# Kernel optimization log

Hardware: AMD Instinct MI355X
Metric: run time of the kernel (lower is better)

Reference implementation:

```python
import jax, jax.numpy as jnp
import numpy as np

N_ENV, N_STEP = 4096, 2048
GAMMA, LAMBDA = 0.99, 0.95


def setup_inputs() -> dict:
    key = jax.random.key(0)
    k1, k2, k3 = jax.random.split(key, 3)
    rewards = jax.random.normal(k1, (N_ENV, N_STEP), dtype=jnp.float32)
    values = jax.random.normal(k2, (N_ENV, N_STEP + 1), dtype=jnp.float32)
    first = (jax.random.uniform(k3, (N_ENV, N_STEP + 1)) < 0.01).astype(jnp.float32)
    return {"rewards": rewards, "values": values, "first": first}


def reference(rewards, values, first):
    """GAE backward recurrence, vectorized over envs via a reverse lax.scan.

    advantages[t] = delta[t] + notlast[t]*gamma*lambda*advantages[t+1]
    delta[t]      = r[t] + notlast[t]*gamma*V[t+1] - V[t]
    """
    notlast = 1.0 - first[:, 1:]                        # [E, T]
    delta = rewards + notlast * GAMMA * values[:, 1:] - values[:, :-1]  # [E, T]

    def step(lastgaelam, xs):
        d_t, nl_t = xs                                  # each [E]
        adv_t = d_t + nl_t * (GAMMA * LAMBDA) * lastgaelam
        return adv_t, adv_t

    init = jnp.zeros(rewards.shape[0], dtype=rewards.dtype)
    _, advs = jax.lax.scan(step, init, (delta.T, notlast.T), reverse=True)
    advantages = advs.T                                 # [E, T]
    v_targ = values[:, :-1] + advantages
    return advantages, v_targ
```

## Files before the change

### kernel.cpp

```cpp
#include <hip/hip_runtime.h>


constexpr int NE   = 4096;
constexpr int NT   = 2048;
constexpr int NT1  = 2049;
constexpr float GAMMA  = 0.99f;
constexpr float LAMBDA = 0.95f;
constexpr int TPB = 256;
constexpr int PER = NT / TPB;
constexpr int NQ  = NT / 4;
constexpr int QPT = NQ / TPB;

typedef float f32x4 __attribute__((ext_vector_type(4)));
typedef float f32x4u __attribute__((ext_vector_type(4), aligned(4)));

__device__ __forceinline__ f32x4 ld4u(const float* p) {
    return (f32x4)*reinterpret_cast<const f32x4u*>(p);
}

__device__ __forceinline__ int swz(int g) { return g ^ ((g >> 3) & 7); }

__global__ __launch_bounds__(TPB) void gae_kernel(
    const float* __restrict__ rewards,
    const float* __restrict__ values,
    const float* __restrict__ first,
    float* __restrict__ out)
{
    __shared__ f32x4 d_lds[NQ];
    __shared__ f32x4 c_lds[NQ];
    __shared__ float sWA[4];
    __shared__ float sWB[4];

    const int e    = blockIdx.x;
    const int tid  = threadIdx.x;
    const int lane = tid & 63;
    const int w    = tid >> 6;

    const float* r_row = rewards + (size_t)e * NT;
    const float* v_row = values  + (size_t)e * NT1;
    const float* f_row = first   + (size_t)e * NT1;

    f32x4 vreg[QPT];
#pragma unroll
    for (int j = 0; j < QPT; ++j) {
        const int q = j * TPB + tid;
        const int t = 4 * q;
        const f32x4 r4  = *reinterpret_cast<const f32x4*>(r_row + t);
        const f32x4 v4a = ld4u(v_row + t);
        const f32x4 v4b = ld4u(v_row + t + 1);
        const f32x4 f4  = ld4u(f_row + t + 1);
        vreg[j] = v4a;
        const f32x4 nl = 1.0f - f4;
        f32x4 d4, c4;
        d4 = r4 + nl * GAMMA * v4b - v4a;
        c4 = nl * (GAMMA * LAMBDA);
        d_lds[swz(q)] = d4;
        c_lds[swz(q)] = c4;
    }
    __syncthreads();

    float d[PER], c[PER];
    {
        const f32x4 da = d_lds[swz(2 * tid)];
        const f32x4 db = d_lds[swz(2 * tid + 1)];
        const f32x4 ca = c_lds[swz(2 * tid)];
        const f32x4 cb = c_lds[swz(2 * tid + 1)];
        d[0]=da.x; d[1]=da.y; d[2]=da.z; d[3]=da.w;
        d[4]=db.x; d[5]=db.y; d[6]=db.z; d[7]=db.w;
        c[0]=ca.x; c[1]=ca.y; c[2]=ca.z; c[3]=ca.w;
        c[4]=cb.x; c[5]=cb.y; c[6]=cb.z; c[7]=cb.w;
    }

    float A = 1.0f, B = 0.0f;
#pragma unroll
    for (int k = PER - 1; k >= 0; --k) {
        B = fmaf(c[k], B, d[k]);
        A *= c[k];
    }

    float cA = A, cB = B;
#pragma unroll
    for (int off = 1; off < 64; off <<= 1) {
        const float a2 = __shfl_down(cA, off);
        const float b2 = __shfl_down(cB, off);
        if (lane + off < 64) {
            cB = fmaf(cA, b2, cB);
            cA = cA * a2;
        }
    }

    if (lane == 0) { sWA[w] = cA; sWB[w] = cB; }

    float EA = __shfl_down(cA, 1);
    float EB = __shfl_down(cB, 1);
    if (lane == 63) { EA = 1.0f; EB = 0.0f; }

    __syncthreads();

    float TB = 0.0f;
    for (int u = 3; u > w; --u) {
        TB = fmaf(sWA[u], TB, sWB[u]);
    }
    float x = fmaf(EA, TB, EB);

    float adv[PER];
#pragma unroll
    for (int k = PER - 1; k >= 0; --k) {
        x = fmaf(c[k], x, d[k]);
        adv[k] = x;
    }
    {
        f32x4 a0; a0.x=adv[0]; a0.y=adv[1]; a0.z=adv[2]; a0.w=adv[3];
        f32x4 a1; a1.x=adv[4]; a1.y=adv[5]; a1.z=adv[6]; a1.w=adv[7];
        d_lds[swz(2 * tid)]     = a0;
        d_lds[swz(2 * tid + 1)] = a1;
    }
    __syncthreads();

    float* __restrict__ adv_out = out + (size_t)e * NT;
    float* __restrict__ vt_out  = out + (size_t)NE * NT + (size_t)e * NT;
#pragma unroll
    for (int j = 0; j < QPT; ++j) {
        const int q = j * TPB + tid;
        const int t = 4 * q;
        const f32x4 a4 = d_lds[swz(q)];
        const f32x4 vt = vreg[j] + a4;
        __builtin_nontemporal_store(a4, reinterpret_cast<f32x4*>(adv_out + t));
        __builtin_nontemporal_store(vt, reinterpret_cast<f32x4*>(vt_out + t));
    }
}

extern "C" void kernel_launch(void* const* d_in, const int* in_sizes, int n_in,
                              void* d_out, int out_size, void* d_ws, size_t ws_size,
                              hipStream_t stream) {
    const float* rewards = (const float*)d_in[0];
    const float* values  = (const float*)d_in[1];
    const float* first   = (const float*)d_in[2];
    float* out = (float*)d_out;
    gae_kernel<<<NE, TPB, 0, stream>>>(rewards, values, first, out);
}
```

Before: 30.01 us.

## Process two envs per block, prefetching second env's loads during first's scan

Each block now handles two environment rows. The second row's global loads are issued before the first row's scan runs, so memory latency overlaps with compute. The shifted values load is replaced by a cross-lane shuffle plus one scalar load for the last lane. __syncthreads is swapped for a raw barrier that waits only on LDS counters. The cost is roughly doubled register pressure from holding the prefetched row, which may lower occupancy, and half as many blocks are launched.

Result: no change. 30.49 us (+1.6%).

```diff
diff --git a/kernel.cpp b/kernel.cpp
--- a/kernel.cpp
+++ b/kernel.cpp
@@ -10,6 +10,8 @@
 constexpr int PER = NT / TPB;
 constexpr int NQ  = NT / 4;
 constexpr int QPT = NQ / TPB;
+constexpr int EPB = 2;
+constexpr int NB  = NE / EPB;
 
 typedef float f32x4 __attribute__((ext_vector_type(4)));
 typedef float f32x4u __attribute__((ext_vector_type(4), aligned(4)));
@@ -20,45 +22,52 @@
 
 __device__ __forceinline__ int swz(int g) { return g ^ ((g >> 3) & 7); }
 
-__global__ __launch_bounds__(TPB) void gae_kernel(
-    const float* __restrict__ rewards,
-    const float* __restrict__ values,
-    const float* __restrict__ first,
-    float* __restrict__ out)
+__device__ __forceinline__ void bar_lds() {
+    asm volatile("s_waitcnt lgkmcnt(0)" ::: "memory");
+    __builtin_amdgcn_sched_barrier(0);
+    __builtin_amdgcn_s_barrier();
+    __builtin_amdgcn_sched_barrier(0);
+}
+
+struct Env { f32x4 r[QPT], v[QPT], f[QPT]; float vn[QPT]; };
+
+__device__ __forceinline__ void load_env(int e, int tid, int lane,
+    const float* __restrict__ rewards, const float* __restrict__ values,
+    const float* __restrict__ first, Env& E)
 {
-    __shared__ f32x4 d_lds[NQ];
-    __shared__ f32x4 c_lds[NQ];
-    __shared__ float sWA[4];
-    __shared__ float sWB[4];
-
-    const int e    = blockIdx.x;
-    const int tid  = threadIdx.x;
-    const int lane = tid & 63;
-    const int w    = tid >> 6;
-
     const float* r_row = rewards + (size_t)e * NT;
     const float* v_row = values  + (size_t)e * NT1;
     const float* f_row = first   + (size_t)e * NT1;
+#pragma unroll
+    for (int j = 0; j < QPT; ++j) {
+        const int t = 4 * (j * TPB + tid);
+        E.r[j] = *reinterpret_cast<const f32x4*>(r_row + t);
+        E.v[j] = ld4u(v_row + t);
+        E.f[j] = ld4u(f_row + t + 1);
+        E.vn[j] = (lane == 63) ? v_row[t + 4] : 0.0f;
+    }
+}
 
-    f32x4 vreg[QPT];
+__device__ __forceinline__ void phase1(const Env& E, int tid, int lane,
+    f32x4* d_lds, f32x4* c_lds, f32x4 vreg[QPT])
+{
 #pragma unroll
     for (int j = 0; j < QPT; ++j) {
         const int q = j * TPB + tid;
-        const int t = 4 * q;
-        const f32x4 r4  = *reinterpret_cast<const f32x4*>(r_row + t);
-        const f32x4 v4a = ld4u(v_row + t);
-        const f32x4 v4b = ld4u(v_row + t + 1);
-        const f32x4 f4  = ld4u(f_row + t + 1);
-        vreg[j] = v4a;
-        const f32x4 nl = 1.0f - f4;
-        f32x4 d4, c4;
-        d4 = r4 + nl * GAMMA * v4b - v4a;
-        c4 = nl * (GAMMA * LAMBDA);
-        d_lds[swz(q)] = d4;
-        c_lds[swz(q)] = c4;
+        float vnext = __shfl_down(E.v[j].x, 1);
+        if (lane == 63) vnext = E.vn[j];
+        f32x4 v4b; v4b.x = E.v[j].y; v4b.y = E.v[j].z; v4b.z = E.v[j].w; v4b.w = vnext;
+        const f32x4 nl = 1.0f - E.f[j];
+        d_lds[swz(q)] = E.r[j] + nl * GAMMA * v4b - E.v[j];
+        c_lds[swz(q)] = nl * (GAMMA * LAMBDA);
+        vreg[j] = E.v[j];
     }
-    __syncthreads();
+}
 
+__device__ __forceinline__ void phase23(int e, int tid, int lane, int w,
+    f32x4* d_lds, f32x4* c_lds, float* sWA, float* sWB,
+    const f32x4 vreg[QPT], float* __restrict__ out)
+{
     float d[PER], c[PER];
     {
         const f32x4 da = d_lds[swz(2 * tid)];
@@ -95,12 +104,10 @@
     float EB = __shfl_down(cB, 1);
     if (lane == 63) { EA = 1.0f; EB = 0.0f; }
 
-    __syncthreads();
+    bar_lds();
 
     float TB = 0.0f;
-    for (int u = 3; u > w; --u) {
-        TB = fmaf(sWA[u], TB, sWB[u]);
-    }
+    for (int u = 3; u > w; --u) TB = fmaf(sWA[u], TB, sWB[u]);
     float x = fmaf(EA, TB, EB);
 
     float adv[PER];
@@ -115,7 +122,7 @@
         d_lds[swz(2 * tid)]     = a0;
         d_lds[swz(2 * tid + 1)] = a1;
     }
-    __syncthreads();
+    bar_lds();
 
     float* __restrict__ adv_out = out + (size_t)e * NT;
     float* __restrict__ vt_out  = out + (size_t)NE * NT + (size_t)e * NT;
@@ -130,6 +137,40 @@
     }
 }
 
+__global__ __launch_bounds__(TPB) void gae_kernel(
+    const float* __restrict__ rewards,
+    const float* __restrict__ values,
+    const float* __restrict__ first,
+    float* __restrict__ out)
+{
+    __shared__ f32x4 d_lds[NQ];
+    __shared__ f32x4 c_lds[NQ];
+    __shared__ float sWA[4];
+    __shared__ float sWB[4];
+
+    const int b    = blockIdx.x;
+    const int tid  = threadIdx.x;
+    const int lane = tid & 63;
+    const int w    = tid >> 6;
+
+    f32x4 vreg0[QPT], vreg1[QPT];
+
+    Env P;
+    load_env(b, tid, lane, rewards, values, first, P);
+    phase1(P, tid, lane, d_lds, c_lds, vreg0);
+
+    Env Q;
+    load_env(b + NB, tid, lane, rewards, values, first, Q);
+
+    bar_lds();
+    phase23(b, tid, lane, w, d_lds, c_lds, sWA, sWB, vreg0, out);
+    bar_lds();
+
+    phase1(Q, tid, lane, d_lds, c_lds, vreg1);
+    bar_lds();
+    phase23(b + NB, tid, lane, w, d_lds, c_lds, sWA, sWB, vreg1, out);
+}
+
 extern "C" void kernel_launch(void* const* d_in, const int* in_sizes, int n_in,
                               void* d_out, int out_size, void* d_ws, size_t ws_size,
                               hipStream_t stream) {
@@ -137,5 +178,5 @@
     const float* values  = (const float*)d_in[1];
     const float* first   = (const float*)d_in[2];
     float* out = (float*)d_out;
-    gae_kernel<<<NE, TPB, 0, stream>>>(rewards, values, first, out);
+    gae_kernel<<<NB, TPB, 0, stream>>>(rewards, values, first, out);
 }
```
